# Performance work log

Measured on AMD Instinct MI355X. Metric: run time of the kernel, lower is better.

Reference implementation:

```python
import jax, jax.numpy as jnp
import numpy as np

K = 5          # kernel_size
PAD = (K - 1) // 2  # fixed_padding with dilation=1, stride=1 -> 'same'


def setup_inputs() -> dict:
    key = jax.random.key(0)
    kx, kw = jax.random.split(key)
    x = jax.random.normal(kx, (4, 8, 512, 512), dtype=jnp.float32)
    # nn.Parameter initialized to zeros in the original; use small random values
    # so the op is non-trivial (math is identical for any weight values).
    weight = jax.random.normal(kw, (8, 8, K, K), dtype=jnp.float32) * 0.05
    return {"x": x, "weight": weight}


def reference(x, weight):
    """Morphological dilation2d with hard max (soft_max=False).

    out[n,o,h,w] = max_{c,dy,dx} ( x_pad[n,c,h+dy,w+dx] + weight[o,c,dy,dx] )
    Faithful to: pad zeros -> unfold -> weight + x -> max over dim C*k*k.
    Computed as a fused sliding-window max-plus reduction (no (N,C,k,k,H,W)
    unfold tensor is materialized; loop is over the fixed k*k kernel taps).
    """
    N, C, H, W = x.shape
    O = weight.shape[0]
    xp = jnp.pad(x, ((0, 0), (0, 0), (PAD, PAD), (PAD, PAD)))  # zero pad, as in F.pad
    out = jnp.full((N, O, H, W), -jnp.inf, dtype=x.dtype)
    for dy in range(K):
        for dx in range(K):
            patch = xp[:, :, dy:dy + H, dx:dx + W]           # (N,C,H,W)
            w_tap = weight[:, :, dy, dx]                      # (O,C)
            # (N,1,C,H,W) + (1,O,C,1,1) -> max over C -> (N,O,H,W)
            term = patch[:, None] + w_tap[None, :, :, None, None]
            out = jnp.maximum(out, jnp.max(term, axis=2))
    return out
```

## Files before the change

kernel.cpp:

```cpp
#include <hip/hip_runtime.h>
#include <math.h>
#include <stdint.h>

typedef _Float16 half2v __attribute__((ext_vector_type(2)));

#define KK 5
#define PADK 2
#define C_IN 8
#define O_OUT 8
#define HH 512
#define WW 512
#define TH 16
#define TW 64
#define LROWS (TH + 2 * PADK)
#define LPAIRS 36
#define NW (O_OUT * C_IN * KK * KK)

static __device__ __forceinline__ half2v bc_h2(uint32_t u) {
    return __builtin_bit_cast(half2v, u);
}
static __device__ __forceinline__ half2v emax(half2v a, half2v b) {
    return __builtin_elementwise_max(a, b);
}

__global__ void prep_weights_kernel(const float* __restrict__ w,
                                    uint32_t* __restrict__ wp) {
    int i = blockIdx.x * 256 + threadIdx.x;
    if (i < NW) {
        _Float16 h = (_Float16)w[i];
        uint16_t hb = __builtin_bit_cast(uint16_t, h);
        wp[i] = ((uint32_t)hb << 16) | (uint32_t)hb;
    }
}

template <bool USE_WS>
__global__ __launch_bounds__(256, 4)
void dil_kernel(const float* __restrict__ x,
                const float* __restrict__ wf,
                const uint32_t* __restrict__ wp,
                float* __restrict__ out) {
    __shared__ uint32_t lds[C_IN][LROWS][LPAIRS];

    const int tid = threadIdx.x;
    const int w0 = blockIdx.x * TW;
    const int h0 = blockIdx.y * TH;
    const int n  = blockIdx.z;

    const float* xn = x + (size_t)n * (C_IN * HH * WW);
    for (int idx = tid; idx < C_IN * LROWS * LPAIRS; idx += 256) {
        int c   = idx / (LROWS * LPAIRS);
        int rem = idx - c * (LROWS * LPAIRS);
        int r   = rem / LPAIRS;
        int jp  = rem - r * LPAIRS;
        int gh = h0 - PADK + r;
        int gw = w0 - PADK + 2 * jp;
        float v0 = 0.f, v1 = 0.f;
        if ((unsigned)gh < (unsigned)HH) {
            const float* row = xn + ((size_t)c * HH + gh) * WW;
            if ((unsigned)gw < (unsigned)WW) v0 = row[gw];
            if ((unsigned)(gw + 1) < (unsigned)WW) v1 = row[gw + 1];
        }
        _Float16 a = (_Float16)v0, b = (_Float16)v1;
        uint32_t u = ((uint32_t)__builtin_bit_cast(uint16_t, b) << 16) |
                     (uint32_t)__builtin_bit_cast(uint16_t, a);
        (&lds[0][0][0])[idx] = u;
    }
    __syncthreads();

    const int tx = tid & 15;
    const int ty = tid >> 4;
    const int pb = 2 * tx;

    const uint32_t NINF = 0xFC00FC00u;
    half2v acc[O_OUT][2];
    #pragma unroll
    for (int o = 0; o < O_OUT; ++o) {
        acc[o][0] = bc_h2(NINF);
        acc[o][1] = bc_h2(NINF);
    }

    for (int c = 0; c < C_IN; ++c) {
        #pragma unroll
        for (int dy = 0; dy < KK; ++dy) {
            const uint32_t* lrow = &lds[c][ty + dy][pb];
            uint2 A = *(const uint2*)lrow;
            uint2 B = *(const uint2*)(lrow + 2);
            uint32_t u0 = A.x, u1 = A.y, u2 = B.x, u3 = B.y;
            uint32_t s0 = (u0 >> 16) | (u1 << 16);
            uint32_t s1 = (u1 >> 16) | (u2 << 16);
            uint32_t s2 = (u2 >> 16) | (u3 << 16);
            half2v H0 = bc_h2(u0), H1 = bc_h2(u1), H2 = bc_h2(u2), H3 = bc_h2(u3);
            half2v S0 = bc_h2(s0), S1 = bc_h2(s1), S2 = bc_h2(s2);

            const int wbase = (c * KK + dy) * KK;
            #pragma unroll
            for (int o = 0; o < O_OUT; ++o) {
                half2v W0, W1, W2, W3, W4;
                const int off = o * (C_IN * KK * KK) + wbase;
                if (USE_WS) {
                    W0 = bc_h2(wp[off + 0]);
                    W1 = bc_h2(wp[off + 1]);
                    W2 = bc_h2(wp[off + 2]);
                    W3 = bc_h2(wp[off + 3]);
                    W4 = bc_h2(wp[off + 4]);
                } else {
                    _Float16 h0w = (_Float16)wf[off + 0];
                    _Float16 h1w = (_Float16)wf[off + 1];
                    _Float16 h2w = (_Float16)wf[off + 2];
                    _Float16 h3w = (_Float16)wf[off + 3];
                    _Float16 h4w = (_Float16)wf[off + 4];
                    W0 = (half2v){h0w, h0w}; W1 = (half2v){h1w, h1w};
                    W2 = (half2v){h2w, h2w}; W3 = (half2v){h3w, h3w};
                    W4 = (half2v){h4w, h4w};
                }
                {
                    half2v t0 = H0 + W0, t1 = S0 + W1, t2 = H1 + W2,
                           t3 = S1 + W3, t4 = H2 + W4;
                    half2v m01 = emax(t0, t1), m23 = emax(t2, t3);
                    acc[o][0] = emax(acc[o][0], emax(emax(m01, m23), t4));
                }
                {
                    half2v t0 = H1 + W0, t1 = S1 + W1, t2 = H2 + W2,
                           t3 = S2 + W3, t4 = H3 + W4;
                    half2v m01 = emax(t0, t1), m23 = emax(t2, t3);
                    acc[o][1] = emax(acc[o][1], emax(emax(m01, m23), t4));
                }
            }
        }
    }

    float* onp = out + (size_t)n * (O_OUT * HH * WW);
    const int h = h0 + ty;
    const int wcol = w0 + 4 * tx;
    #pragma unroll
    for (int o = 0; o < O_OUT; ++o) {
        float4 r;
        r.x = (float)acc[o][0].x;
        r.y = (float)acc[o][0].y;
        r.z = (float)acc[o][1].x;
        r.w = (float)acc[o][1].y;
        *(float4*)(&onp[((size_t)o * HH + h) * WW + wcol]) = r;
    }
}

extern "C" void kernel_launch(void* const* d_in, const int* in_sizes, int n_in,
                              void* d_out, int out_size, void* d_ws, size_t ws_size,
                              hipStream_t stream) {
    const float* x   = (const float*)d_in[0];
    const float* wgt = (const float*)d_in[1];
    float* out = (float*)d_out;

    dim3 grid(WW / TW, HH / TH, 4);
    dim3 block(256);

    if (ws_size >= (size_t)NW * 4) {
        uint32_t* wp = (uint32_t*)d_ws;
        prep_weights_kernel<<<(NW + 255) / 256, 256, 0, stream>>>(wgt, wp);
        dil_kernel<true><<<grid, block, 0, stream>>>(x, wgt, wp, out);
    } else {
        dil_kernel<false><<<grid, block, 0, stream>>>(x, wgt, nullptr, out);
    }
}
```

Measured before the change: 79.15 us.

## Halve tile height and per-thread outputs, reorder packed weights for contiguous loads

Reduces the tile to 8 rows and gives each thread 2 output pixels instead of 4, so accumulator registers drop and launch bounds can target 8 waves per SIMD. Packed weights are reordered to (c,dy,o,dx) so a tap row's weights for all outputs sit contiguously for scalar loads. The trade-off is a larger halo fraction (12 loaded rows per 8 output rows), less register reuse of LDS data per thread, and narrower float2 stores.

```diff
diff --git a/kernel.cpp b/kernel.cpp
--- a/kernel.cpp
+++ b/kernel.cpp
@@ -10,7 +10,7 @@
 #define O_OUT 8
 #define HH 512
 #define WW 512
-#define TH 16
+#define TH 8
 #define TW 64
 #define LROWS (TH + 2 * PADK)
 #define LPAIRS 36
@@ -27,14 +27,20 @@
                                     uint32_t* __restrict__ wp) {
     int i = blockIdx.x * 256 + threadIdx.x;
     if (i < NW) {
+        int dx = i % KK;
+        int t  = i / KK;
+        int dy = t % KK;  t /= KK;
+        int c  = t % C_IN;
+        int o  = t / C_IN;
         _Float16 h = (_Float16)w[i];
         uint16_t hb = __builtin_bit_cast(uint16_t, h);
-        wp[i] = ((uint32_t)hb << 16) | (uint32_t)hb;
+        int j = ((c * KK + dy) * O_OUT + o) * KK + dx;
+        wp[j] = ((uint32_t)hb << 16) | (uint32_t)hb;
     }
 }
 
 template <bool USE_WS>
-__global__ __launch_bounds__(256, 4)
+__global__ __launch_bounds__(256, 8)
 void dil_kernel(const float* __restrict__ x,
                 const float* __restrict__ wf,
                 const uint32_t* __restrict__ wp,
@@ -67,43 +73,39 @@
     }
     __syncthreads();
 
-    const int tx = tid & 15;
-    const int ty = tid >> 4;
-    const int pb = 2 * tx;
+    const int tx = tid & 31;
+    const int ty = tid >> 5;
 
     const uint32_t NINF = 0xFC00FC00u;
-    half2v acc[O_OUT][2];
+    half2v acc[O_OUT];
     #pragma unroll
-    for (int o = 0; o < O_OUT; ++o) {
-        acc[o][0] = bc_h2(NINF);
-        acc[o][1] = bc_h2(NINF);
-    }
+    for (int o = 0; o < O_OUT; ++o) acc[o] = bc_h2(NINF);
 
     for (int c = 0; c < C_IN; ++c) {
         #pragma unroll
         for (int dy = 0; dy < KK; ++dy) {
-            const uint32_t* lrow = &lds[c][ty + dy][pb];
-            uint2 A = *(const uint2*)lrow;
-            uint2 B = *(const uint2*)(lrow + 2);
-            uint32_t u0 = A.x, u1 = A.y, u2 = B.x, u3 = B.y;
+            const uint32_t* lrow = &lds[c][ty + dy][tx];
+            uint32_t u0 = lrow[0];
+            uint32_t u1 = lrow[1];
+            uint32_t u2 = lrow[2];
             uint32_t s0 = (u0 >> 16) | (u1 << 16);
             uint32_t s1 = (u1 >> 16) | (u2 << 16);
-            uint32_t s2 = (u2 >> 16) | (u3 << 16);
-            half2v H0 = bc_h2(u0), H1 = bc_h2(u1), H2 = bc_h2(u2), H3 = bc_h2(u3);
-            half2v S0 = bc_h2(s0), S1 = bc_h2(s1), S2 = bc_h2(s2);
+            half2v H0 = bc_h2(u0), H1 = bc_h2(u1), H2 = bc_h2(u2);
+            half2v S0 = bc_h2(s0), S1 = bc_h2(s1);
 
-            const int wbase = (c * KK + dy) * KK;
+            const int wbase = (c * KK + dy) * (O_OUT * KK);
             #pragma unroll
             for (int o = 0; o < O_OUT; ++o) {
                 half2v W0, W1, W2, W3, W4;
-                const int off = o * (C_IN * KK * KK) + wbase;
                 if (USE_WS) {
+                    const int off = wbase + o * KK;
                     W0 = bc_h2(wp[off + 0]);
                     W1 = bc_h2(wp[off + 1]);
                     W2 = bc_h2(wp[off + 2]);
                     W3 = bc_h2(wp[off + 3]);
                     W4 = bc_h2(wp[off + 4]);
                 } else {
+                    const int off = ((o * C_IN + c) * KK + dy) * KK;
                     _Float16 h0w = (_Float16)wf[off + 0];
                     _Float16 h1w = (_Float16)wf[off + 1];
                     _Float16 h2w = (_Float16)wf[off + 2];
@@ -113,33 +115,23 @@
                     W2 = (half2v){h2w, h2w}; W3 = (half2v){h3w, h3w};
                     W4 = (half2v){h4w, h4w};
                 }
-                {
-                    half2v t0 = H0 + W0, t1 = S0 + W1, t2 = H1 + W2,
-                           t3 = S1 + W3, t4 = H2 + W4;
-                    half2v m01 = emax(t0, t1), m23 = emax(t2, t3);
-                    acc[o][0] = emax(acc[o][0], emax(emax(m01, m23), t4));
-                }
-                {
-                    half2v t0 = H1 + W0, t1 = S1 + W1, t2 = H2 + W2,
-                           t3 = S2 + W3, t4 = H3 + W4;
-                    half2v m01 = emax(t0, t1), m23 = emax(t2, t3);
-                    acc[o][1] = emax(acc[o][1], emax(emax(m01, m23), t4));
-                }
+                half2v t0 = H0 + W0, t1 = S0 + W1, t2 = H1 + W2,
+                       t3 = S1 + W3, t4 = H2 + W4;
+                half2v m01 = emax(t0, t1), m23 = emax(t2, t3);
+                acc[o] = emax(acc[o], emax(emax(m01, m23), t4));
             }
         }
     }
 
     float* onp = out + (size_t)n * (O_OUT * HH * WW);
     const int h = h0 + ty;
-    const int wcol = w0 + 4 * tx;
+    const int wcol = w0 + 2 * tx;
     #pragma unroll
     for (int o = 0; o < O_OUT; ++o) {
-        float4 r;
-        r.x = (float)acc[o][0].x;
-        r.y = (float)acc[o][0].y;
-        r.z = (float)acc[o][1].x;
-        r.w = (float)acc[o][1].y;
-        *(float4*)(&onp[((size_t)o * HH + h) * WW + wcol]) = r;
+        float2 r;
+        r.x = (float)acc[o].x;
+        r.y = (float)acc[o].y;
+        *(float2*)(&onp[((size_t)o * HH + h) * WW + wcol]) = r;
     }
 }
 
```

New measurement: 74.98 us. 1.06x faster.
